# Optimization experiments

Hardware: AMD Instinct MI355X
Metric: run time of the kernel (lower is better)

## Reference

```python
import jax, jax.numpy as jnp
import numpy as np

EPS = 1e-12  # F.normalize default eps

def l2norm(x, axis=1):
    n = jnp.sqrt(jnp.sum(x * x, axis=axis, keepdims=True))
    return x / jnp.maximum(n, EPS)

def setup_inputs() -> dict:
    key = jax.random.key(0)
    ks = jax.random.split(key, 8)
    N, C, H, W = 32, 1024, 28, 28
    D, K, OUT = 128, 64, 1024
    return {
        "x": jax.random.normal(ks[0], (N, C, H, W), dtype=jnp.float32),
        "Wpool": jax.random.normal(ks[1], (D, C), dtype=jnp.float32) * 0.02,
        "bpool": jax.random.normal(ks[2], (D,), dtype=jnp.float32) * 0.02,
        "Wconv": jax.random.normal(ks[3], (K, D), dtype=jnp.float32) * 0.1,
        "bconv": jax.random.normal(ks[4], (K,), dtype=jnp.float32) * 0.02,
        "centroids": jax.random.uniform(ks[5], (K, D), dtype=jnp.float32),
        "Wproj": jax.random.normal(ks[6], (OUT, K * D), dtype=jnp.float32) * 0.02,
        "bproj": jax.random.normal(ks[7], (OUT,), dtype=jnp.float32) * 0.02,
    }

def reference(x, Wpool, bpool, Wconv, bconv, centroids, Wproj, bproj):
    N, C, H, W = x.shape
    K, D = centroids.shape
    S = H * W
    # 1x1 conv channel pool: (N,C,H,W) -> (N,D,H,W)
    x = jnp.einsum('nchw,dc->ndhw', x, Wpool) + bpool[None, :, None, None]
    # descriptor-wise L2 norm over channel dim
    x = l2norm(x, axis=1)
    xf = x.reshape(N, D, S)                      # (N,D,S)
    # 1x1 conv -> soft assignment logits, softmax over clusters
    sa = jnp.einsum('nds,kd->nks', xf, Wconv) + bconv[None, :, None]
    sa = jax.nn.softmax(sa, axis=1)              # (N,K,S)
    # vlad[n,k,d] = sum_s sa[n,k,s]*(xf[n,d,s] - centroids[k,d])
    #            = (sa @ xf^T) - centroids * sum_s sa   (GEMM rewrite, same math)
    vlad = jnp.einsum('nks,nds->nkd', sa, xf) - centroids[None] * jnp.sum(sa, axis=-1)[:, :, None]
    vlad = l2norm(vlad, axis=1)                  # L2Norm over dim=1 (clusters)
    vlad = vlad.reshape(N, K * D)
    vlad = vlad @ Wproj.T + bproj
    return l2norm(vlad, axis=1)
```

## Files before the change

### kernel.cpp

```cpp
#include <hip/hip_runtime.h>
#include <math.h>

#define NB 32
#define CC 1024
#define SS 784
#define SP 832
#define DD 128
#define KK 64
#define OUTD 1024
#define KD 8192
#define PSPLIT 16

#define OFF_XN    0
#define OFF_SA    (OFF_XN + NB*DD*SP*2)
#define OFF_WPK   (OFF_SA + NB*KK*SP*2)
#define OFF_WCK   (OFF_WPK + 32*8*64*8*2)
#define OFF_VLADN (OFF_WCK + 16*64*8*2)
#define OFF_OUTP  (OFF_VLADN + NB*KD*4)

typedef __attribute__((ext_vector_type(8))) short bf16x8;
typedef __attribute__((ext_vector_type(4))) float f32x4;
typedef __attribute__((ext_vector_type(4))) unsigned int u32x4;

__device__ __forceinline__ unsigned int pk_bf16(float a, float b) {
    unsigned int ua = __builtin_bit_cast(unsigned int, a);
    unsigned int ub = __builtin_bit_cast(unsigned int, b);
    ua += 0x7FFFu + ((ua >> 16) & 1u);
    ub += 0x7FFFu + ((ub >> 16) & 1u);
    return (ua >> 16) | (ub & 0xFFFF0000u);
}
__device__ __forceinline__ unsigned short f2bf(float a) {
    unsigned int ua = __builtin_bit_cast(unsigned int, a);
    ua += 0x7FFFu + ((ua >> 16) & 1u);
    return (unsigned short)(ua >> 16);
}
__device__ __forceinline__ float bf2f(unsigned short u) {
    unsigned int v = ((unsigned int)u) << 16;
    return __builtin_bit_cast(float, v);
}


__global__ __launch_bounds__(256)
void pack_weights(const float* __restrict__ Wpool, const float* __restrict__ Wconv,
                  unsigned short* __restrict__ Wpk, unsigned short* __restrict__ Wck)
{
    const int b = blockIdx.x;
    const int t = threadIdx.x;
    if (b < 8) {
        const int i = blockIdx.y;
        const int id = t + 256 * i;
        const int ktl = id >> 9;
        const int mt  = (id >> 6) & 7;
        const int l   = id & 63;
        const int lm = l & 15, quad = l >> 4;
        const int kt = b * 4 + ktl;
        const int d = mt * 16 + lm;
        const int cb = kt * 4 + quad;
        const int base_c = (cb >> 5) * 256 + ((cb >> 3) & 3) * 64 + (cb & 7);
        float v[8];
#pragma unroll
        for (int j = 0; j < 8; j++) v[j] = Wpool[(size_t)d * CC + base_c + 8 * j];
        unsigned int* dst = (unsigned int*)&Wpk[(size_t)((kt * 8 + mt) * 64 + l) * 8];
        dst[0] = pk_bf16(v[0], v[1]); dst[1] = pk_bf16(v[2], v[3]);
        dst[2] = pk_bf16(v[4], v[5]); dst[3] = pk_bf16(v[6], v[7]);
    } else if (blockIdx.y < 4) {
        const int i = blockIdx.y;
        const int id = t + 256 * i;
        const int tile = id >> 6;
        const int l = id & 63;
        const int lm = l & 15, quad = l >> 4;
        const int k = (tile >> 2) * 16 + lm;
        const int d = (tile & 3) * 32 + quad * 8;
        const float4 v0 = *(const float4*)&Wconv[(size_t)k * DD + d];
        const float4 v1 = *(const float4*)&Wconv[(size_t)k * DD + d + 4];
        unsigned int* dst = (unsigned int*)&Wck[(size_t)(tile * 64 + l) * 8];
        dst[0] = pk_bf16(v0.x, v0.y); dst[1] = pk_bf16(v0.z, v0.w);
        dst[2] = pk_bf16(v1.x, v1.y); dst[3] = pk_bf16(v1.z, v1.w);
    }
}

__global__ __launch_bounds__(256, 4)
void pool_norm_assign(const float* __restrict__ x, const unsigned short* __restrict__ Wpk,
                      const float* __restrict__ bpool, const unsigned short* __restrict__ Wck,
                      const float* __restrict__ bconv,
                      unsigned short* __restrict__ xn, unsigned short* __restrict__ sa)
{
    const int n  = blockIdx.y;
    const int s0 = blockIdx.x * 32;
    const int t  = threadIdx.x;
    const int l  = t & 63;
    const int w  = t >> 6;
    const int lm = l & 15;
    const int quad = l >> 4;

    __shared__ alignas(16) unsigned char smem[2 * 32 * 32 * 8 * 2 + 4 * 32 * 4];
    unsigned short* Bst0 = (unsigned short*)smem;
    unsigned short* Bst1 = Bst0 + 32 * 32 * 8;
    unsigned short* xnT  = Bst0;
    float* red  = (float*)(smem + 2 * 32 * 32 * 8 * 2);
    float* sums = red;

    unsigned short* xnp = xn + (size_t)n * DD * SP;
    unsigned short* sap = sa + (size_t)n * KK * SP;

    if (s0 >= SS) {
        const u32x4 z = (u32x4){0u, 0u, 0u, 0u};
#pragma unroll
        for (int pp = 0; pp < 2; pp++) {
            const int idx = t + 256 * pp;
            *(u32x4*)&xnp[(size_t)(idx >> 2) * SP + s0 + (idx & 3) * 8] = z;
        }
        *(u32x4*)&sap[(size_t)(t >> 2) * SP + s0 + (t & 3) * 8] = z;
        return;
    }

    const int r0 = (l >> 3) & 7;
    const int se = l & 7;
    int sc = s0 + se * 4;
    if (sc + 4 > SS) sc = s0 + (se & 3) * 4;
    const float* xw = x + (size_t)n * CC * SS + sc;
    const int crow0 = w * 64 + r0;

    f32x4 g[8];
#pragma unroll
    for (int j = 0; j < 8; j++)
        g[j] = *(const f32x4*)&xw[(size_t)(crow0 + j * 8) * SS];

    bf16x8 abuf[4][2];
#pragma unroll
    for (int p = 0; p < 4; p++)
#pragma unroll
        for (int i = 0; i < 2; i++)
            abuf[p][i] = *(const bf16x8*)&Wpk[(size_t)((p * 8 + w * 2 + i) * 64 + l) * 8];

    __builtin_amdgcn_sched_barrier(0);

#pragma unroll
    for (int ss = 0; ss < 4; ss++) {
        const int s = se * 4 + ss;
        const int sig = s ^ ((s >> 3) & 3);
        unsigned int* dst = (unsigned int*)&Bst0[(size_t)((w * 8 + r0) * 32 + sig) * 8];
        dst[0] = pk_bf16(g[0][ss], g[1][ss]); dst[1] = pk_bf16(g[2][ss], g[3][ss]);
        dst[2] = pk_bf16(g[4][ss], g[5][ss]); dst[3] = pk_bf16(g[6][ss], g[7][ss]);
    }
    __syncthreads();

    f32x4 acc[2][2];
#pragma unroll
    for (int i = 0; i < 2; i++)
#pragma unroll
        for (int h = 0; h < 2; h++) acc[i][h] = (f32x4){0.f, 0.f, 0.f, 0.f};

    for (int q = 0; q < 4; ++q) {
        if (q < 3) {
#pragma unroll
            for (int j = 0; j < 8; j++)
                g[j] = *(const f32x4*)&xw[(size_t)((q + 1) * 256 + crow0 + j * 8) * SS];
        }
        __builtin_amdgcn_sched_barrier(0);
        const unsigned short* Bq = (q & 1) ? Bst1 : Bst0;
#pragma unroll
        for (int ktq = 0; ktq < 8; ++ktq) {
            const int kt = q * 8 + ktq;
            const bf16x8 a0 = abuf[ktq & 3][0], a1 = abuf[ktq & 3][1];
            if (kt < 28) {
#pragma unroll
                for (int i = 0; i < 2; i++)
                    abuf[ktq & 3][i] = *(const bf16x8*)&Wpk[(size_t)(((kt + 4) * 8 + w * 2 + i) * 64 + l) * 8];
            }
#pragma unroll
            for (int h = 0; h < 2; h++) {
                const int s = h * 16 + lm;
                const int sig = s ^ ((s >> 3) & 3);
                const bf16x8 bf = *(const bf16x8*)&Bq[(size_t)((ktq * 4 + quad) * 32 + sig) * 8];
                acc[0][h] = __builtin_amdgcn_mfma_f32_16x16x32_bf16(a0, bf, acc[0][h], 0, 0, 0);
                acc[1][h] = __builtin_amdgcn_mfma_f32_16x16x32_bf16(a1, bf, acc[1][h], 0, 0, 0);
            }
        }
        __builtin_amdgcn_sched_barrier(0);
        if (q < 3) {
            unsigned short* Bn = ((q + 1) & 1) ? Bst1 : Bst0;
#pragma unroll
            for (int ss = 0; ss < 4; ss++) {
                const int s = se * 4 + ss;
                const int sig = s ^ ((s >> 3) & 3);
                unsigned int* dst = (unsigned int*)&Bn[(size_t)((w * 8 + r0) * 32 + sig) * 8];
                dst[0] = pk_bf16(g[0][ss], g[1][ss]); dst[1] = pk_bf16(g[2][ss], g[3][ss]);
                dst[2] = pk_bf16(g[4][ss], g[5][ss]); dst[3] = pk_bf16(g[6][ss], g[7][ss]);
            }
        }
        __syncthreads();
    }

    float vals[2][2][4];
    float ssq[2] = {0.f, 0.f};
#pragma unroll
    for (int i = 0; i < 2; i++)
#pragma unroll
        for (int h = 0; h < 2; h++)
#pragma unroll
            for (int r = 0; r < 4; r++) {
                const int d = (w * 2 + i) * 16 + quad * 4 + r;
                const float v = acc[i][h][r] + bpool[d];
                vals[i][h][r] = v; ssq[h] += v * v;
            }
#pragma unroll
    for (int h = 0; h < 2; h++) {
        ssq[h] += __shfl_xor(ssq[h], 16, 64);
        ssq[h] += __shfl_xor(ssq[h], 32, 64);
    }
    if (quad == 0) { red[w * 32 + lm] = ssq[0]; red[w * 32 + 16 + lm] = ssq[1]; }
    __syncthreads();
    float scale[2];
#pragma unroll
    for (int h = 0; h < 2; h++) {
        const int sl = h * 16 + lm;
        scale[h] = 1.f / fmaxf(sqrtf(red[0 * 32 + sl] + red[1 * 32 + sl] + red[2 * 32 + sl] + red[3 * 32 + sl]), 1e-12f);
    }
#pragma unroll
    for (int i = 0; i < 2; i++)
#pragma unroll
        for (int h = 0; h < 2; h++)
#pragma unroll
            for (int r = 0; r < 4; r++) {
                const int d = (w * 2 + i) * 16 + quad * 4 + r;
                const int sg = s0 + h * 16 + lm;
                const float v = vals[i][h][r] * scale[h];
                xnp[(size_t)d * SP + sg] = f2bf(v);
                xnT[(size_t)(((d >> 3) * 32) + h * 16 + lm) * 8 + (d & 7)] = f2bf(v);
            }
    __syncthreads();

    f32x4 acc2[2];
    acc2[0] = (f32x4){0.f, 0.f, 0.f, 0.f};
    acc2[1] = (f32x4){0.f, 0.f, 0.f, 0.f};
#pragma unroll
    for (int dsv = 0; dsv < 4; dsv++) {
        const bf16x8 afrag = *(const bf16x8*)&Wck[(size_t)((w * 4 + dsv) * 64 + l) * 8];
#pragma unroll
        for (int h = 0; h < 2; h++) {
            const bf16x8 bfrag = *(const bf16x8*)&xnT[(size_t)((dsv * 4 + quad) * 32 + h * 16 + lm) * 8];
            acc2[h] = __builtin_amdgcn_mfma_f32_16x16x32_bf16(afrag, bfrag, acc2[h], 0, 0, 0);
        }
    }
    float e[2][4]; float ps[2] = {0.f, 0.f};
#pragma unroll
    for (int h = 0; h < 2; h++)
#pragma unroll
        for (int r = 0; r < 4; r++) {
            const int k = w * 16 + quad * 4 + r;
            e[h][r] = expf(acc2[h][r] + bconv[k]);
            ps[h] += e[h][r];
        }
#pragma unroll
    for (int h = 0; h < 2; h++) {
        ps[h] += __shfl_xor(ps[h], 16, 64);
        ps[h] += __shfl_xor(ps[h], 32, 64);
    }
    if (quad == 0) { sums[w * 32 + lm] = ps[0]; sums[w * 32 + 16 + lm] = ps[1]; }
    __syncthreads();
#pragma unroll
    for (int h = 0; h < 2; h++) {
        const int sl = h * 16 + lm;
        const int sg = s0 + sl;
        const float inv = 1.f / (sums[0 * 32 + sl] + sums[1 * 32 + sl] + sums[2 * 32 + sl] + sums[3 * 32 + sl]);
        const bool val2 = sg < SS;
#pragma unroll
        for (int r = 0; r < 4; r++) {
            const int k = w * 16 + quad * 4 + r;
            sap[(size_t)k * SP + sg] = val2 ? f2bf(e[h][r] * inv) : (unsigned short)0;
        }
    }
}

__global__ __launch_bounds__(256)
void vlad_full(const unsigned short* __restrict__ xn, const unsigned short* __restrict__ sa,
               const float* __restrict__ centroids, float* __restrict__ vladn)
{
    const int dg = blockIdx.x;
    const int n  = blockIdx.y;
    const int t  = threadIdx.x;
    const int l  = t & 63;
    const int w  = t >> 6;
    const int lm = l & 15, quad = l >> 4;

    __shared__ float sas[KK];
    __shared__ float red[4][16];

    const unsigned short* sap = sa + (size_t)n * KK * SP + (size_t)(w * 16 + lm) * SP + quad * 8;
    const unsigned short* xnp = xn + (size_t)n * DD * SP + (size_t)(dg * 16 + lm) * SP + quad * 8;

    f32x4 acc = (f32x4){0.f, 0.f, 0.f, 0.f};
    float ssum = 0.f;

    bf16x8 afA, bfA, afB, bfB;
    afA = *(const bf16x8*)&sap[0];
    bfA = *(const bf16x8*)&xnp[0];
    afB = *(const bf16x8*)&sap[32];
    bfB = *(const bf16x8*)&xnp[32];
    __builtin_amdgcn_sched_barrier(0);

#pragma unroll
    for (int st = 0; st < 26; st += 2) {
        const bf16x8 a0 = afA, b0 = bfA;
        if (st + 2 < 26) {
            afA = *(const bf16x8*)&sap[(st + 2) * 32];
            bfA = *(const bf16x8*)&xnp[(st + 2) * 32];
        }
        acc = __builtin_amdgcn_mfma_f32_16x16x32_bf16(a0, b0, acc, 0, 0, 0);
#pragma unroll
        for (int j = 0; j < 8; j++) ssum += bf2f((unsigned short)a0[j]);

        const bf16x8 a1 = afB, b1 = bfB;
        if (st + 3 < 26) {
            afB = *(const bf16x8*)&sap[(st + 3) * 32];
            bfB = *(const bf16x8*)&xnp[(st + 3) * 32];
        }
        acc = __builtin_amdgcn_mfma_f32_16x16x32_bf16(a1, b1, acc, 0, 0, 0);
#pragma unroll
        for (int j = 0; j < 8; j++) ssum += bf2f((unsigned short)a1[j]);
    }

    ssum += __shfl_xor(ssum, 16, 64);
    ssum += __shfl_xor(ssum, 32, 64);
    if (quad == 0) sas[w * 16 + lm] = ssum;
    __syncthreads();

    float v[4]; float ssq = 0.f;
    const int d = dg * 16 + lm;
#pragma unroll
    for (int r = 0; r < 4; r++) {
        const int k = w * 16 + quad * 4 + r;
        v[r] = acc[r] - centroids[(size_t)k * DD + d] * sas[k];
        ssq += v[r] * v[r];
    }
    ssq += __shfl_xor(ssq, 16, 64);
    ssq += __shfl_xor(ssq, 32, 64);
    if (quad == 0) red[w][lm] = ssq;
    __syncthreads();
    const float tot = red[0][lm] + red[1][lm] + red[2][lm] + red[3][lm];
    const float scale = 1.f / fmaxf(sqrtf(tot), 1e-12f);

    float* vo = vladn + (size_t)n * KD;
#pragma unroll
    for (int r = 0; r < 4; r++) {
        const int k = w * 16 + quad * 4 + r;
        vo[(size_t)k * DD + d] = v[r] * scale;
    }
}

#define PROJ_ISSUE(L, KT) do {                                              \
    const int c_ = (KT) * 32;                                               \
    L[0] = *(const f32x4*)&wrow[c_];  L[1] = *(const f32x4*)&wrow[c_ + 4];  \
    L[2] = *(const f32x4*)&arow0[c_]; L[3] = *(const f32x4*)&arow0[c_ + 4]; \
    L[4] = *(const f32x4*)&arow1[c_]; L[5] = *(const f32x4*)&arow1[c_ + 4]; \
} while (0)

#define PROJ_STEP(L) do {                                                    \
    union { unsigned int u[4]; bf16x8 v; } ub, ua0, ua1;                     \
    ub.u[0]  = pk_bf16(L[0][0], L[0][1]); ub.u[1]  = pk_bf16(L[0][2], L[0][3]); \
    ub.u[2]  = pk_bf16(L[1][0], L[1][1]); ub.u[3]  = pk_bf16(L[1][2], L[1][3]); \
    ua0.u[0] = pk_bf16(L[2][0], L[2][1]); ua0.u[1] = pk_bf16(L[2][2], L[2][3]); \
    ua0.u[2] = pk_bf16(L[3][0], L[3][1]); ua0.u[3] = pk_bf16(L[3][2], L[3][3]); \
    ua1.u[0] = pk_bf16(L[4][0], L[4][1]); ua1.u[1] = pk_bf16(L[4][2], L[4][3]); \
    ua1.u[2] = pk_bf16(L[5][0], L[5][1]); ua1.u[3] = pk_bf16(L[5][2], L[5][3]); \
    acc[0] = __builtin_amdgcn_mfma_f32_16x16x32_bf16(ua0.v, ub.v, acc[0], 0, 0, 0); \
    acc[1] = __builtin_amdgcn_mfma_f32_16x16x32_bf16(ua1.v, ub.v, acc[1], 0, 0, 0); \
} while (0)

__global__ __launch_bounds__(256)
void proj_mfma(const float* __restrict__ vladn, const float* __restrict__ Wproj,
               float* __restrict__ outp)
{
    const int o0 = blockIdx.x * 64;
    const int c0 = blockIdx.y * (KD / PSPLIT);
    const int t  = threadIdx.x;
    const int l  = t & 63;
    const int w  = t >> 6;
    const int lm = l & 15, quad = l >> 4;
    const int o  = o0 + w * 16 + lm;

    const float* wrow  = &Wproj[(size_t)o * KD + c0 + quad * 8];
    const float* arow0 = &vladn[(size_t)lm * KD + c0 + quad * 8];
    const float* arow1 = &vladn[(size_t)(16 + lm) * KD + c0 + quad * 8];

    f32x4 acc[2];
    acc[0] = (f32x4){0.f, 0.f, 0.f, 0.f};
    acc[1] = (f32x4){0.f, 0.f, 0.f, 0.f};

    f32x4 LA[6], LB[6];
    PROJ_ISSUE(LA, 0);
#pragma unroll
    for (int kt = 0; kt < 16; kt += 2) {
        PROJ_ISSUE(LB, kt + 1);
        __builtin_amdgcn_sched_barrier(0);
        PROJ_STEP(LA);
        if (kt + 2 < 16) PROJ_ISSUE(LA, kt + 2);
        __builtin_amdgcn_sched_barrier(0);
        PROJ_STEP(LB);
    }

#pragma unroll
    for (int a = 0; a < 2; a++)
#pragma unroll
        for (int r = 0; r < 4; r++) {
            const int nn = a * 16 + quad * 4 + r;
            outp[((size_t)blockIdx.y * NB + nn) * OUTD + o] = acc[a][r];
        }
}

__global__ __launch_bounds__(256)
void final_norm_kernel(const float* __restrict__ outp, const float* __restrict__ bproj,
                       float* __restrict__ out)
{
    const int n = blockIdx.x;
    const int t = threadIdx.x;
    const int o4 = t * 4;

    float4 a = *(const float4*)&bproj[o4];
    f32x4 pr[PSPLIT];
#pragma unroll
    for (int i = 0; i < PSPLIT; i++)
        pr[i] = *(const f32x4*)&outp[((size_t)i * NB + n) * OUTD + o4];
    __builtin_amdgcn_sched_barrier(0);
#pragma unroll
    for (int i = 0; i < PSPLIT; i++) {
        a.x += pr[i][0]; a.y += pr[i][1]; a.z += pr[i][2]; a.w += pr[i][3];
    }
    float ssp = a.x * a.x + a.y * a.y + a.z * a.z + a.w * a.w;
#pragma unroll
    for (int off = 32; off > 0; off >>= 1) ssp += __shfl_down(ssp, off, 64);
    __shared__ float rs[4];
    if ((t & 63) == 0) rs[t >> 6] = ssp;
    __syncthreads();
    const float total = rs[0] + rs[1] + rs[2] + rs[3];
    const float scale = 1.f / fmaxf(sqrtf(total), 1e-12f);
    float4 o;
    o.x = a.x * scale; o.y = a.y * scale; o.z = a.z * scale; o.w = a.w * scale;
    *(float4*)&out[(size_t)n * OUTD + o4] = o;
}

extern "C" void kernel_launch(void* const* d_in, const int* in_sizes, int n_in,
                              void* d_out, int out_size, void* d_ws, size_t ws_size,
                              hipStream_t stream)
{
    const float* x         = (const float*)d_in[0];
    const float* Wpool     = (const float*)d_in[1];
    const float* bpool     = (const float*)d_in[2];
    const float* Wconv     = (const float*)d_in[3];
    const float* bconv     = (const float*)d_in[4];
    const float* centroids = (const float*)d_in[5];
    const float* Wproj     = (const float*)d_in[6];
    const float* bproj     = (const float*)d_in[7];
    float* out = (float*)d_out;
    char*  wsb = (char*)d_ws;

    unsigned short* xn     = (unsigned short*)(wsb + OFF_XN);
    unsigned short* sa     = (unsigned short*)(wsb + OFF_SA);
    unsigned short* Wpk    = (unsigned short*)(wsb + OFF_WPK);
    unsigned short* Wck    = (unsigned short*)(wsb + OFF_WCK);
    float*          vladn  = (float*)(wsb + OFF_VLADN);
    float*          outp   = (float*)(wsb + OFF_OUTP);

    pack_weights<<<dim3(9, 8), 256, 0, stream>>>(Wpool, Wconv, Wpk, Wck);
    pool_norm_assign<<<dim3(26, NB), 256, 0, stream>>>(x, Wpk, bpool, Wck, bconv, xn, sa);
    vlad_full<<<dim3(DD / 16, NB), 256, 0, stream>>>(xn, sa, centroids, vladn);
    proj_mfma<<<dim3(OUTD / 64, PSPLIT), 256, 0, stream>>>(vladn, Wproj, outp);
    final_norm_kernel<<<dim3(NB), 256, 0, stream>>>(outp, bproj, out);
}
```

Before: 216.5 us.

## Split VLAD reduction over spatial halves and double projection K-split

The vlad_full kernel now launches 512 threads and splits the spatial reduction into two halves of 13 steps each. The second half's partial accumulators and assignment sums are combined through shared memory before normalization. The projection split-K factor goes from 16 to 32, halving each block's K loop and doubling the number of blocks. The final norm kernel now reads 32 partials in two batches. The aim is more parallelism and latency hiding in small-grid kernels, at the cost of extra shared-memory syncs and more partial-sum traffic.

```diff
diff --git a/kernel.cpp b/kernel.cpp
--- a/kernel.cpp
+++ b/kernel.cpp
@@ -9,7 +9,7 @@
 #define KK 64
 #define OUTD 1024
 #define KD 8192
-#define PSPLIT 16
+#define PSPLIT 32
 
 #define OFF_XN    0
 #define OFF_SA    (OFF_XN + NB*DD*SP*2)
@@ -273,7 +273,7 @@
     }
 }
 
-__global__ __launch_bounds__(256)
+__global__ __launch_bounds__(512)
 void vlad_full(const unsigned short* __restrict__ xn, const unsigned short* __restrict__ sa,
                const float* __restrict__ centroids, float* __restrict__ vladn)
 {
@@ -281,14 +281,18 @@
     const int n  = blockIdx.y;
     const int t  = threadIdx.x;
     const int l  = t & 63;
-    const int w  = t >> 6;
+    const int w8 = t >> 6;
+    const int kt = w8 & 3;
+    const int sh = w8 >> 2;
     const int lm = l & 15, quad = l >> 4;
 
     __shared__ float sas[KK];
     __shared__ float red[4][16];
-
-    const unsigned short* sap = sa + (size_t)n * KK * SP + (size_t)(w * 16 + lm) * SP + quad * 8;
-    const unsigned short* xnp = xn + (size_t)n * DD * SP + (size_t)(dg * 16 + lm) * SP + quad * 8;
+    __shared__ alignas(16) float accb[4][64][4];
+    __shared__ float ssb[4][16];
+
+    const unsigned short* sap = sa + (size_t)n * KK * SP + (size_t)(kt * 16 + lm) * SP + sh * 13 * 32 + quad * 8;
+    const unsigned short* xnp = xn + (size_t)n * DD * SP + (size_t)(dg * 16 + lm) * SP + sh * 13 * 32 + quad * 8;
 
     f32x4 acc = (f32x4){0.f, 0.f, 0.f, 0.f};
     float ssum = 0.f;
@@ -301,9 +305,9 @@
     __builtin_amdgcn_sched_barrier(0);
 
 #pragma unroll
-    for (int st = 0; st < 26; st += 2) {
+    for (int st = 0; st < 13; st += 2) {
         const bf16x8 a0 = afA, b0 = bfA;
-        if (st + 2 < 26) {
+        if (st + 2 < 13) {
             afA = *(const bf16x8*)&sap[(st + 2) * 32];
             bfA = *(const bf16x8*)&xnp[(st + 2) * 32];
         }
@@ -311,41 +315,58 @@
 #pragma unroll
         for (int j = 0; j < 8; j++) ssum += bf2f((unsigned short)a0[j]);
 
-        const bf16x8 a1 = afB, b1 = bfB;
-        if (st + 3 < 26) {
-            afB = *(const bf16x8*)&sap[(st + 3) * 32];
-            bfB = *(const bf16x8*)&xnp[(st + 3) * 32];
-        }
-        acc = __builtin_amdgcn_mfma_f32_16x16x32_bf16(a1, b1, acc, 0, 0, 0);
-#pragma unroll
-        for (int j = 0; j < 8; j++) ssum += bf2f((unsigned short)a1[j]);
+        if (st + 1 < 13) {
+            const bf16x8 a1 = afB, b1 = bfB;
+            if (st + 3 < 13) {
+                afB = *(const bf16x8*)&sap[(st + 3) * 32];
+                bfB = *(const bf16x8*)&xnp[(st + 3) * 32];
+            }
+            acc = __builtin_amdgcn_mfma_f32_16x16x32_bf16(a1, b1, acc, 0, 0, 0);
+#pragma unroll
+            for (int j = 0; j < 8; j++) ssum += bf2f((unsigned short)a1[j]);
+        }
     }
 
     ssum += __shfl_xor(ssum, 16, 64);
     ssum += __shfl_xor(ssum, 32, 64);
-    if (quad == 0) sas[w * 16 + lm] = ssum;
-    __syncthreads();
-
-    float v[4]; float ssq = 0.f;
-    const int d = dg * 16 + lm;
-#pragma unroll
-    for (int r = 0; r < 4; r++) {
-        const int k = w * 16 + quad * 4 + r;
-        v[r] = acc[r] - centroids[(size_t)k * DD + d] * sas[k];
-        ssq += v[r] * v[r];
-    }
-    ssq += __shfl_xor(ssq, 16, 64);
-    ssq += __shfl_xor(ssq, 32, 64);
-    if (quad == 0) red[w][lm] = ssq;
-    __syncthreads();
-    const float tot = red[0][lm] + red[1][lm] + red[2][lm] + red[3][lm];
-    const float scale = 1.f / fmaxf(sqrtf(tot), 1e-12f);
-
-    float* vo = vladn + (size_t)n * KD;
-#pragma unroll
-    for (int r = 0; r < 4; r++) {
-        const int k = w * 16 + quad * 4 + r;
-        vo[(size_t)k * DD + d] = v[r] * scale;
+
+    if (sh == 1) {
+        *(f32x4*)&accb[kt][l][0] = acc;
+        if (quad == 0) ssb[kt][lm] = ssum;
+    }
+    __syncthreads();
+
+    float v[4];
+    if (sh == 0) {
+        const f32x4 p = *(const f32x4*)&accb[kt][l][0];
+        acc += p;
+        ssum += ssb[kt][lm];
+        if (quad == 0) sas[kt * 16 + lm] = ssum;
+
+        float ssq = 0.f;
+        const int d = dg * 16 + lm;
+#pragma unroll
+        for (int r = 0; r < 4; r++) {
+            const int k = kt * 16 + quad * 4 + r;
+            v[r] = acc[r] - centroids[(size_t)k * DD + d] * sas[k];
+            ssq += v[r] * v[r];
+        }
+        ssq += __shfl_xor(ssq, 16, 64);
+        ssq += __shfl_xor(ssq, 32, 64);
+        if (quad == 0) red[kt][lm] = ssq;
+    }
+    __syncthreads();
+
+    if (sh == 0) {
+        const int d = dg * 16 + lm;
+        const float tot = red[0][lm] + red[1][lm] + red[2][lm] + red[3][lm];
+        const float scale = 1.f / fmaxf(sqrtf(tot), 1e-12f);
+        float* vo = vladn + (size_t)n * KD;
+#pragma unroll
+        for (int r = 0; r < 4; r++) {
+            const int k = kt * 16 + quad * 4 + r;
+            vo[(size_t)k * DD + d] = v[r] * scale;
+        }
     }
 }
 
@@ -391,11 +412,11 @@
     f32x4 LA[6], LB[6];
     PROJ_ISSUE(LA, 0);
 #pragma unroll
-    for (int kt = 0; kt < 16; kt += 2) {
+    for (int kt = 0; kt < 8; kt += 2) {
         PROJ_ISSUE(LB, kt + 1);
         __builtin_amdgcn_sched_barrier(0);
         PROJ_STEP(LA);
-        if (kt + 2 < 16) PROJ_ISSUE(LA, kt + 2);
+        if (kt + 2 < 8) PROJ_ISSUE(LA, kt + 2);
         __builtin_amdgcn_sched_barrier(0);
         PROJ_STEP(LB);
     }
@@ -418,14 +439,17 @@
     const int o4 = t * 4;
 
     float4 a = *(const float4*)&bproj[o4];
-    f32x4 pr[PSPLIT];
-#pragma unroll
-    for (int i = 0; i < PSPLIT; i++)
-        pr[i] = *(const f32x4*)&outp[((size_t)i * NB + n) * OUTD + o4];
-    __builtin_amdgcn_sched_barrier(0);
-#pragma unroll
-    for (int i = 0; i < PSPLIT; i++) {
-        a.x += pr[i][0]; a.y += pr[i][1]; a.z += pr[i][2]; a.w += pr[i][3];
+    f32x4 pr[16];
+#pragma unroll
+    for (int b = 0; b < 2; b++) {
+#pragma unroll
+        for (int i = 0; i < 16; i++)
+            pr[i] = *(const f32x4*)&outp[((size_t)(b * 16 + i) * NB + n) * OUTD + o4];
+        __builtin_amdgcn_sched_barrier(0);
+#pragma unroll
+        for (int i = 0; i < 16; i++) {
+            a.x += pr[i][0]; a.y += pr[i][1]; a.z += pr[i][2]; a.w += pr[i][3];
+        }
     }
     float ssp = a.x * a.x + a.y * a.y + a.z * a.z + a.w * a.w;
 #pragma unroll
@@ -464,7 +488,7 @@
 
     pack_weights<<<dim3(9, 8), 256, 0, stream>>>(Wpool, Wconv, Wpk, Wck);
     pool_norm_assign<<<dim3(26, NB), 256, 0, stream>>>(x, Wpk, bpool, Wck, bconv, xn, sa);
-    vlad_full<<<dim3(DD / 16, NB), 256, 0, stream>>>(xn, sa, centroids, vladn);
+    vlad_full<<<dim3(DD / 16, NB), 512, 0, stream>>>(xn, sa, centroids, vladn);
     proj_mfma<<<dim3(OUTD / 64, PSPLIT), 256, 0, stream>>>(vladn, Wproj, outp);
     final_norm_kernel<<<dim3(NB), 256, 0, stream>>>(outp, bproj, out);
 }
```

Result: no change. 216.8 us (+0.1%).
